# Kernel optimization log

Hardware: AMD Instinct MI355X
Metric: run time of the kernel (lower is better)

The kernel has to match this reference:

```python
import jax, jax.numpy as jnp
import numpy as np

C = 64
HW = 21 * 21  # 441
NEIGHBOR_K = 3


def setup_inputs() -> dict:
    key = jax.random.key(0)
    k1, k2, k3, k4 = jax.random.split(key, 4)
    B1, B2 = 32, 25
    x1 = jax.random.normal(k1, (B1, C, 21, 21), dtype=jnp.float32)
    x2 = jax.random.normal(k2, (B2, C, 21, 21), dtype=jnp.float32)
    mask1 = jax.random.uniform(k3, (B1, 21, 21), dtype=jnp.float32)
    mask2 = jax.random.uniform(k4, (B2, 21, 21), dtype=jnp.float32)
    return {"x1": x1, "x2": x2, "mask1": mask1, "mask2": mask2}


def reference(x1, x2, mask1, mask2):
    B1 = x1.shape[0]
    B2 = x2.shape[0]
    q = x1.reshape(B1, C, HW)  # (B1, 64, 441) query descriptors
    s = x2.reshape(B2, C, HW)  # (B2, 64, 441) support descriptors
    # per-descriptor L2 norms over channel dim
    qn = jnp.linalg.norm(q, axis=1)  # (B1, 441)
    sn = jnp.linalg.norm(s, axis=1)  # (B2, 441)
    # cosine similarity between every query descriptor and every support descriptor
    inner = jnp.einsum('aci,bcj->abij', q, s)  # (B1, B2, 441, 441)
    sim = inner / (qn[:, None, :, None] * sn[None, :, None, :])
    # mask out invalid spatial positions on both sides
    sim = sim * mask1.reshape(B1, 1, HW, 1) * mask2.reshape(1, B2, 1, HW)
    # top-k nearest support descriptors per query descriptor, sum over all
    topk_vals, _ = jax.lax.top_k(sim, NEIGHBOR_K)  # (B1, B2, 441, k)
    return topk_vals.reshape(B1, B2, -1).sum(axis=2)  # (B1, B2)
```

## Files before the change

kernel.cpp:

```cpp
#include <hip/hip_runtime.h>
#include <math.h>

#define CCH 64
#define HW 441
#define HWP 448
#define NT 28
#define NB2 25
#define TPB 256
#define PANEL (HWP * CCH)

typedef _Float16 half8 __attribute__((ext_vector_type(8)));
typedef float f32x4 __attribute__((ext_vector_type(4)));

__global__ void normalize_frag_kernel(const float* __restrict__ x1,
                                      const float* __restrict__ m1,
                                      const float* __restrict__ x2,
                                      const float* __restrict__ m2,
                                      _Float16* __restrict__ qh,
                                      _Float16* __restrict__ sh,
                                      int n1rows, int nrows) {
    int idx = blockIdx.x * blockDim.x + threadIdx.x;
    if (idx >= nrows) return;
    const float* x; const float* mk; _Float16* outp; int rb;
    if (idx < n1rows) { x = x1; mk = m1; outp = qh; rb = idx; }
    else             { x = x2; mk = m2; outp = sh; rb = idx - n1rows; }
    int b = rb / HWP, i = rb - b * HWP;
    float vals[CCH];
    if (i < HW) {
        const float* xb = x + (size_t)b * CCH * HW + i;
        float ss = 0.f;
#pragma unroll
        for (int c = 0; c < CCH; ++c) { float v = xb[c * HW]; vals[c] = v; ss += v * v; }
        float scale = mk[b * HW + i] * rsqrtf(ss);
#pragma unroll
        for (int c = 0; c < CCH; ++c) vals[c] *= scale;
    } else {
#pragma unroll
        for (int c = 0; c < CCH; ++c) vals[c] = 0.f;
    }
    _Float16* pb = outp + (size_t)b * PANEL + (i >> 4) * 1024 + (i & 15) * 8;
#pragma unroll
    for (int f = 0; f < 2; ++f) {
#pragma unroll
        for (int qd = 0; qd < 4; ++qd) {
            half8 h;
#pragma unroll
            for (int e = 0; e < 8; ++e) h[e] = (_Float16)vals[f * 32 + qd * 8 + e];
            *(half8*)(pb + f * 512 + qd * 128) = h;
        }
    }
}

#define TOP3_INSERT(v, t0, t1, t2)        \
    do {                                  \
        float _m = fmaxf(t0, v);          \
        float _c = fminf(t0, v);          \
        t0 = _m;                          \
        _m = fmaxf(t1, _c);               \
        _c = fminf(t1, _c);               \
        t1 = _m;                          \
        t2 = fmaxf(t2, _c);               \
    } while (0)

#define MERGE3(t0, t1, t2, b0, b1, b2)            \
    do {                                          \
        float _m0 = fmaxf(t0, b0);                \
        float _n0 = fminf(t0, b0);                \
        float _m1 = fmaxf(t1, b1);                \
        float _t2 = fmaxf(t2, b2);                \
        t0 = _m0;                                 \
        t1 = fmaxf(_n0, _m1);                     \
        t2 = fmaxf(fminf(_n0, _m1), _t2);         \
    } while (0)

template <int NI>
__device__ __forceinline__ float do_pass(const _Float16* __restrict__ qpanel,
                                         const _Float16* __restrict__ spanel,
                                         int it0, int lane, int quad) {
    const float NEG = -1e30f;
    half8 bf0[NI], bf1[NI];
#pragma unroll
    for (int t = 0; t < NI; ++t) {
        const _Float16* qp = qpanel + (it0 + t) * 1024 + lane * 8;
        bf0[t] = *(const half8*)qp;
        bf1[t] = *(const half8*)(qp + 512);
    }
    float t0[NI], t1[NI], t2[NI];
#pragma unroll
    for (int t = 0; t < NI; ++t) { t0[t] = NEG; t1[t] = NEG; t2[t] = NEG; }

    for (int jt = 0; jt < NT; ++jt) {
        const _Float16* sp = spanel + jt * 1024 + lane * 8;
        half8 a0 = *(const half8*)sp;
        half8 a1 = *(const half8*)(sp + 512);
        f32x4 acc[NI];
#pragma unroll
        for (int t = 0; t < NI; ++t) {
            f32x4 z = {0.f, 0.f, 0.f, 0.f};
            z = __builtin_amdgcn_mfma_f32_16x16x32_f16(a0, bf0[t], z, 0, 0, 0);
            z = __builtin_amdgcn_mfma_f32_16x16x32_f16(a1, bf1[t], z, 0, 0, 0);
            acc[t] = z;
        }
        if (jt == NT - 1) {
#pragma unroll
            for (int t = 0; t < NI; ++t) {
#pragma unroll
                for (int r = 0; r < 4; ++r)
                    if (quad * 4 + r >= 9) acc[t][r] = NEG;
            }
        }
#pragma unroll
        for (int t = 0; t < NI; ++t) {
#pragma unroll
            for (int r = 0; r < 4; ++r)
                TOP3_INSERT(acc[t][r], t0[t], t1[t], t2[t]);
        }
    }

    float res = 0.f;
#pragma unroll
    for (int t = 0; t < NI; ++t) {
        float b0 = __shfl_xor(t0[t], 16), b1 = __shfl_xor(t1[t], 16), b2 = __shfl_xor(t2[t], 16);
        MERGE3(t0[t], t1[t], t2[t], b0, b1, b2);
        b0 = __shfl_xor(t0[t], 32); b1 = __shfl_xor(t1[t], 32); b2 = __shfl_xor(t2[t], 32);
        MERGE3(t0[t], t1[t], t2[t], b0, b1, b2);
        res += t0[t] + t1[t] + t2[t];
    }
    return (quad == 0) ? res : 0.f;
}

__global__ __launch_bounds__(TPB) void sim_topk_mfma(const _Float16* __restrict__ qh,
                                                     const _Float16* __restrict__ sh,
                                                     float* __restrict__ out) {
    __shared__ float s_red[4];
    int pair = blockIdx.x;
    int a = pair / NB2, b = pair - a * NB2;
    int tid = threadIdx.x, wave = tid >> 6, lane = tid & 63, quad = lane >> 4;
    const _Float16* qpanel = qh + (size_t)a * PANEL;
    const _Float16* spanel = sh + (size_t)b * PANEL;

    float wacc = do_pass<4>(qpanel, spanel, wave * 7, lane, quad)
               + do_pass<3>(qpanel, spanel, wave * 7 + 4, lane, quad);

#pragma unroll
    for (int off = 32; off > 0; off >>= 1) wacc += __shfl_down(wacc, off);
    if (lane == 0) s_red[wave] = wacc;
    __syncthreads();
    if (tid == 0) out[pair] = s_red[0] + s_red[1] + s_red[2] + s_red[3];
}

extern "C" void kernel_launch(void* const* d_in, const int* in_sizes, int n_in,
                              void* d_out, int out_size, void* d_ws, size_t ws_size,
                              hipStream_t stream) {
    const float* x1 = (const float*)d_in[0];
    const float* x2 = (const float*)d_in[1];
    const float* m1 = (const float*)d_in[2];
    const float* m2 = (const float*)d_in[3];
    float* out = (float*)d_out;

    int B1 = in_sizes[0] / (CCH * HW);
    int B2 = in_sizes[1] / (CCH * HW);

    _Float16* qh = (_Float16*)d_ws;
    _Float16* sh = qh + (size_t)B1 * PANEL;

    int n1 = B1 * HWP, ntot = (B1 + B2) * HWP;
    normalize_frag_kernel<<<(ntot + TPB - 1) / TPB, TPB, 0, stream>>>(
        x1, m1, x2, m2, qh, sh, n1, ntot);
    sim_topk_mfma<<<B1 * B2, TPB, 0, stream>>>(qh, sh, out);
}
```

Baseline: 116.1 us.

## Split each pair across four blocks, divergent wave paths, and vectorised top-3 merge

Each (query,support) pair is now spread over four 128-thread blocks, each taking 7 query tiles, and the partial sums are combined with atomicAdd into an output zeroed by a memset. Each wave runs a single pass, wave 0 with 4 tiles and wave 1 with 3, where before every wave ran both passes serially. The aim is more blocks, better occupancy and a shorter serial chain per wave. The per-element top-3 insertion is replaced by a sort-of-4 followed by a merge, which cuts compare ops, and the last-tile masking is peeled out of the main loop. The cost is atomics, an extra memset launch, and float summation order that is no longer deterministic.

```diff
diff --git a/kernel.cpp b/kernel.cpp
--- a/kernel.cpp
+++ b/kernel.cpp
@@ -6,7 +6,6 @@
 #define HWP 448
 #define NT 28
 #define NB2 25
-#define TPB 256
 #define PANEL (HWP * CCH)
 
 typedef _Float16 half8 __attribute__((ext_vector_type(8)));
@@ -51,16 +50,20 @@
     }
 }
 
-#define TOP3_INSERT(v, t0, t1, t2)        \
-    do {                                  \
-        float _m = fmaxf(t0, v);          \
-        float _c = fminf(t0, v);          \
-        t0 = _m;                          \
-        _m = fmaxf(t1, _c);               \
-        _c = fminf(t1, _c);               \
-        t1 = _m;                          \
-        t2 = fmaxf(t2, _c);               \
-    } while (0)
+__device__ __forceinline__ void top3of4_merge(f32x4 v, float& t0, float& t1, float& t2) {
+    float s1 = fmaxf(v[0], v[1]), n1 = fminf(v[0], v[1]);
+    float s2 = fmaxf(v[2], v[3]), n2 = fminf(v[2], v[3]);
+    float x = fminf(s1, s2), y = fmaxf(n1, n2);
+    float b0 = fmaxf(s1, s2);
+    float b1 = fmaxf(x, y);
+    float b2 = fminf(x, y);
+    float m0 = fmaxf(t0, b0), nn0 = fminf(t0, b0);
+    float m1 = fmaxf(t1, b1);
+    float mt2 = fmaxf(t2, b2);
+    t0 = m0;
+    t1 = fmaxf(nn0, m1);
+    t2 = fmaxf(fminf(nn0, m1), mt2);
+}
 
 #define MERGE3(t0, t1, t2, b0, b1, b2)            \
     do {                                          \
@@ -74,14 +77,15 @@
     } while (0)
 
 template <int NI>
-__device__ __forceinline__ float do_pass(const _Float16* __restrict__ qpanel,
+__device__ __forceinline__ float do_pass(const _Float16* __restrict__ qtiles,
                                          const _Float16* __restrict__ spanel,
-                                         int it0, int lane, int quad) {
+                                         int lane, int quad) {
     const float NEG = -1e30f;
+    const f32x4 FZ = {0.f, 0.f, 0.f, 0.f};
     half8 bf0[NI], bf1[NI];
 #pragma unroll
     for (int t = 0; t < NI; ++t) {
-        const _Float16* qp = qpanel + (it0 + t) * 1024 + lane * 8;
+        const _Float16* qp = qtiles + t * 1024 + lane * 8;
         bf0[t] = *(const half8*)qp;
         bf1[t] = *(const half8*)(qp + 512);
     }
@@ -89,31 +93,29 @@
 #pragma unroll
     for (int t = 0; t < NI; ++t) { t0[t] = NEG; t1[t] = NEG; t2[t] = NEG; }
 
-    for (int jt = 0; jt < NT; ++jt) {
+    for (int jt = 0; jt < NT - 1; ++jt) {
         const _Float16* sp = spanel + jt * 1024 + lane * 8;
         half8 a0 = *(const half8*)sp;
         half8 a1 = *(const half8*)(sp + 512);
-        f32x4 acc[NI];
 #pragma unroll
         for (int t = 0; t < NI; ++t) {
-            f32x4 z = {0.f, 0.f, 0.f, 0.f};
-            z = __builtin_amdgcn_mfma_f32_16x16x32_f16(a0, bf0[t], z, 0, 0, 0);
+            f32x4 z = __builtin_amdgcn_mfma_f32_16x16x32_f16(a0, bf0[t], FZ, 0, 0, 0);
             z = __builtin_amdgcn_mfma_f32_16x16x32_f16(a1, bf1[t], z, 0, 0, 0);
-            acc[t] = z;
+            top3of4_merge(z, t0[t], t1[t], t2[t]);
         }
-        if (jt == NT - 1) {
-#pragma unroll
-            for (int t = 0; t < NI; ++t) {
-#pragma unroll
-                for (int r = 0; r < 4; ++r)
-                    if (quad * 4 + r >= 9) acc[t][r] = NEG;
-            }
-        }
+    }
+    {
+        const _Float16* sp = spanel + (NT - 1) * 1024 + lane * 8;
+        half8 a0 = *(const half8*)sp;
+        half8 a1 = *(const half8*)(sp + 512);
 #pragma unroll
         for (int t = 0; t < NI; ++t) {
+            f32x4 z = __builtin_amdgcn_mfma_f32_16x16x32_f16(a0, bf0[t], FZ, 0, 0, 0);
+            z = __builtin_amdgcn_mfma_f32_16x16x32_f16(a1, bf1[t], z, 0, 0, 0);
 #pragma unroll
             for (int r = 0; r < 4; ++r)
-                TOP3_INSERT(acc[t][r], t0[t], t1[t], t2[t]);
+                if (quad * 4 + r >= 9) z[r] = NEG;
+            top3of4_merge(z, t0[t], t1[t], t2[t]);
         }
     }
 
@@ -129,24 +131,26 @@
     return (quad == 0) ? res : 0.f;
 }
 
-__global__ __launch_bounds__(TPB) void sim_topk_mfma(const _Float16* __restrict__ qh,
-                                                     const _Float16* __restrict__ sh,
-                                                     float* __restrict__ out) {
-    __shared__ float s_red[4];
-    int pair = blockIdx.x;
+__global__ __launch_bounds__(128, 6) void sim_topk_mfma(const _Float16* __restrict__ qh,
+                                                        const _Float16* __restrict__ sh,
+                                                        float* __restrict__ out) {
+    __shared__ float s_red[2];
+    int blk = blockIdx.x;
+    int pair = blk >> 2, g = blk & 3;
     int a = pair / NB2, b = pair - a * NB2;
     int tid = threadIdx.x, wave = tid >> 6, lane = tid & 63, quad = lane >> 4;
-    const _Float16* qpanel = qh + (size_t)a * PANEL;
+    const _Float16* qtiles = qh + (size_t)a * PANEL + (size_t)g * 7 * 1024;
     const _Float16* spanel = sh + (size_t)b * PANEL;
 
-    float wacc = do_pass<4>(qpanel, spanel, wave * 7, lane, quad)
-               + do_pass<3>(qpanel, spanel, wave * 7 + 4, lane, quad);
+    float wacc = (wave == 0)
+                     ? do_pass<4>(qtiles, spanel, lane, quad)
+                     : do_pass<3>(qtiles + 4 * 1024, spanel, lane, quad);
 
 #pragma unroll
     for (int off = 32; off > 0; off >>= 1) wacc += __shfl_down(wacc, off);
     if (lane == 0) s_red[wave] = wacc;
     __syncthreads();
-    if (tid == 0) out[pair] = s_red[0] + s_red[1] + s_red[2] + s_red[3];
+    if (tid == 0) atomicAdd(&out[pair], s_red[0] + s_red[1]);
 }
 
 extern "C" void kernel_launch(void* const* d_in, const int* in_sizes, int n_in,
@@ -164,8 +168,10 @@
     _Float16* qh = (_Float16*)d_ws;
     _Float16* sh = qh + (size_t)B1 * PANEL;
 
+    hipMemsetAsync(d_out, 0, (size_t)out_size * sizeof(float), stream);
+
     int n1 = B1 * HWP, ntot = (B1 + B2) * HWP;
-    normalize_frag_kernel<<<(ntot + TPB - 1) / TPB, TPB, 0, stream>>>(
+    normalize_frag_kernel<<<(ntot + 255) / 256, 256, 0, stream>>>(
         x1, m1, x2, m2, qh, sh, n1, ntot);
-    sim_topk_mfma<<<B1 * B2, TPB, 0, stream>>>(qh, sh, out);
+    sim_topk_mfma<<<B1 * B2 * 4, 128, 0, stream>>>(qh, sh, out);
 }
```

Result: faster. 107.4 us (-7.5%).
